# Kernel tuning notes

Measured on AMD Instinct MI355X. Metric: run time of the kernel, lower is better.

The kernel has to match this reference:

```python
import jax, jax.numpy as jnp
import numpy as np

NUM_ROUTING = 3


def squash(s, axis=-1):
    # squash(s) = |s|^2/(1+|s|^2) * s/|s|  (no epsilon, matching the torch code)
    sq = jnp.sum(s * s, axis=axis, keepdims=True)
    return sq / (1.0 + sq) * (s / jnp.sqrt(sq))


def setup_inputs() -> dict:
    key = jax.random.key(0)
    k1, k2 = jax.random.split(key)
    B, in_dim, in_num = 256, 8, 1152
    out_num, out_dim = 10, 16
    x = jax.random.normal(k1, (B, in_dim, in_num), dtype=jnp.float32)
    W = jax.random.normal(k2, (in_num, out_num, out_dim, in_dim), dtype=jnp.float32)
    return {"x": x, "W": W}


def reference(x, W):
    # x: [B, in_dim, in_num]; W: [in_num(i), out_num(j), out_dim(d), in_dim(c)]
    B = x.shape[0]
    in_num, out_num = W.shape[0], W.shape[1]
    # u_hat[i,j,b,d] = sum_c W[i,j,d,c] * x[b,c,i]
    u_hat = jnp.einsum('ijdc,bci->ijbd', W, x)
    b_ij = jnp.zeros((in_num, out_num), dtype=x.dtype)
    v = None
    for _ in range(NUM_ROUTING):
        # DGL reduce: softmax over the output-capsule axis (bucket dim)
        c = jax.nn.softmax(b_ij, axis=1)                    # [i, j]
        s = jnp.einsum('ij,ijbd->jbd', c, u_hat)            # [j, B, d]
        v = squash(s, axis=2)                               # [j, B, d]
        # edge update: b_ij += mean_b sum_d v[j,b,d] * u_hat[i,j,b,d]
        b_ij = b_ij + jnp.einsum('jbd,ijbd->ij', v, u_hat) / B
    # output: [B, out_num, out_dim, 1]
    return jnp.transpose(v, (1, 0, 2))[..., None]
```

## Files before the change

kernel.cpp:

```cpp
#include <hip/hip_runtime.h>

#define IN_NUM 1152
#define OUT_NUM 10
#define OUT_DIM 16
#define IN_DIM 8
#define NB 256
#define KTOT 9216

#define OFF_SPART 0
#define SZ_SPART (96 * OUT_NUM * OUT_DIM * NB)
#define OFF_BP (OFF_SPART + SZ_SPART)
#define SZ_BP (32 * IN_NUM * OUT_NUM)
#define OFF_VT (OFF_BP + SZ_BP)
#define SZ_VT (NB * OUT_NUM * OUT_DIM)
#define OFF_WT2 (OFF_VT + SZ_VT)
#define SZ_WT2 (OUT_NUM * KTOT * OUT_DIM)
#define OFF_WTBF (OFF_WT2 + SZ_WT2)
#define SZ_WTBF (OUT_NUM * OUT_DIM * KTOT / 2)
#define OFF_XBF (OFF_WTBF + SZ_WTBF)
#define SZ_XBF (NB * KTOT / 2)

typedef short bf16x8 __attribute__((ext_vector_type(8)));
typedef float f32x4 __attribute__((ext_vector_type(4)));

__device__ __forceinline__ unsigned short f2bf(float f) {
    unsigned u = __float_as_uint(f);
    u = (u + 0x7FFFu + ((u >> 16) & 1u)) >> 16;
    return (unsigned short)u;
}
__device__ __forceinline__ float bf2f(unsigned short h) {
    return __uint_as_float((unsigned)h << 16);
}

__global__ __launch_bounds__(256) void k_prep(const float* __restrict__ x,
                                              const float* __restrict__ W,
                                              float* __restrict__ Wt2,
                                              unsigned short* __restrict__ Wtbf,
                                              unsigned short* __restrict__ xbf) {
    int u = blockIdx.x, t = threadIdx.x;
    if (u < 360) {
        __shared__ float lds2[32][129];
        int itile = u / 10, j = u - itile * 10;
        int i0 = itile * 32;
        int r0 = t >> 5, c4b = t & 31;
#pragma unroll
        for (int rr = 0; rr < 4; ++rr) {
            int rrow = rr * 8 + r0;
            float4 w4 = *reinterpret_cast<const float4*>(
                &W[(size_t)(i0 + rrow) * 1280 + j * 128 + c4b * 4]);
            lds2[rrow][c4b * 4 + 0] = w4.x; lds2[rrow][c4b * 4 + 1] = w4.y;
            lds2[rrow][c4b * 4 + 2] = w4.z; lds2[rrow][c4b * 4 + 3] = w4.w;
        }
        __syncthreads();
        int ii = t & 31, dcq = t >> 5;
#pragma unroll
        for (int rr = 0; rr < 16; ++rr) {
            int dc = rr * 8 + dcq;
            Wtbf[(size_t)(j * 128 + dc) * IN_NUM + i0 + ii] = f2bf(lds2[ii][dc]);
        }
        int d4 = t & 3, ii2 = (t >> 2) & 31, ch0 = t >> 7;
#pragma unroll
        for (int c2 = 0; c2 < 4; ++c2) {
            int c = c2 * 2 + ch0;
            float4 o;
            o.x = lds2[ii2][(d4 * 4 + 0) * 8 + c];
            o.y = lds2[ii2][(d4 * 4 + 1) * 8 + c];
            o.z = lds2[ii2][(d4 * 4 + 2) * 8 + c];
            o.w = lds2[ii2][(d4 * 4 + 3) * 8 + c];
            *reinterpret_cast<float4*>(
                &Wt2[((size_t)j * KTOT + c * IN_NUM + i0 + ii2) * OUT_DIM + d4 * 4]) = o;
        }
    } else {
        int u2 = u - 360;
        const float4* x4 = reinterpret_cast<const float4*>(x);
#pragma unroll
        for (int p = 0; p < 16; ++p) {
            int e4 = u2 * 4096 + p * 256 + t;
            float4 v = x4[e4];
            ushort4 o;
            o.x = f2bf(v.x); o.y = f2bf(v.y); o.z = f2bf(v.z); o.w = f2bf(v.w);
            *reinterpret_cast<ushort4*>(&xbf[(size_t)e4 * 4]) = o;
        }
    }
}

__global__ __launch_bounds__(256, 4) void k_p1(const float* __restrict__ x,
                                               const float* __restrict__ Wt2,
                                               const float* __restrict__ bp,
                                               float* __restrict__ spart, int it) {
    __shared__ float ldc[96];
    __shared__ unsigned short atT[16][100];
    int w = blockIdx.x, t = threadIdx.x;
    int g8 = w / 80, r = w - g8 * 80;
    int j = r >> 3, isp = g8 * 8 + (r & 7);
    int cch = isp / 12;
    int i0 = (isp - cch * 12) * 96;
    int k0 = isp * 96;
    if (t < 96) {
        float cv;
        if (it == 0) {
            cv = 0.1f;
        } else {
            int i = i0 + t;
            float bt_[OUT_NUM];
#pragma unroll
            for (int jp = 0; jp < OUT_NUM; ++jp) bt_[jp] = 0.f;
#pragma unroll 4
            for (int row = 0; row < 32; ++row) {
                const float2* p2 = reinterpret_cast<const float2*>(
                    &bp[(size_t)row * (IN_NUM * OUT_NUM) + i * OUT_NUM]);
#pragma unroll
                for (int q = 0; q < 5; ++q) {
                    float2 v = p2[q];
                    bt_[q * 2] += v.x; bt_[q * 2 + 1] += v.y;
                }
            }
            float m = -1e30f;
#pragma unroll
            for (int jp = 0; jp < OUT_NUM; ++jp) { bt_[jp] *= (1.f / NB); m = fmaxf(m, bt_[jp]); }
            float s = 0.f;
#pragma unroll
            for (int jp = 0; jp < OUT_NUM; ++jp) { bt_[jp] = __expf(bt_[jp] - m); s += bt_[jp]; }
            cv = bt_[j] / s;
        }
        ldc[t] = cv;
    }
    __syncthreads();
    for (int e = t; e < 1536; e += 256) {
        int d = e & 15, kk = e >> 4;
        atT[d][kk] = f2bf(ldc[kk] * Wt2[((size_t)j * KTOT + k0 + kk) * OUT_DIM + d]);
    }
    __syncthreads();
    int lane = t & 63, wv = t >> 6;
    int lg = lane >> 4, lm = lane & 15;
    bf16x8 bfr[3];
#pragma unroll
    for (int ks = 0; ks < 3; ++ks) {
        const unsigned short* p0 = &atT[lm][ks * 32 + lg * 4];
        ushort4 u0 = *reinterpret_cast<const ushort4*>(p0);
        ushort4 u1 = *reinterpret_cast<const ushort4*>(p0 + 16);
        bfr[ks][0] = (short)u0.x; bfr[ks][1] = (short)u0.y;
        bfr[ks][2] = (short)u0.z; bfr[ks][3] = (short)u0.w;
        bfr[ks][4] = (short)u1.x; bfr[ks][5] = (short)u1.y;
        bfr[ks][6] = (short)u1.z; bfr[ks][7] = (short)u1.w;
    }
    float* sp = spart + ((size_t)isp * OUT_NUM + j) * (OUT_DIM * NB);
#pragma unroll
    for (int tb = 0; tb < 4; ++tb) {
        int tbase = (wv * 4 + tb) * 16;
        const float* xr = x + (size_t)(tbase + lm) * KTOT + k0 + lg * 4;
        f32x4 acc = {0.f, 0.f, 0.f, 0.f};
#pragma unroll
        for (int ks = 0; ks < 3; ++ks) {
            float4 a0 = *reinterpret_cast<const float4*>(xr + ks * 32);
            float4 a1 = *reinterpret_cast<const float4*>(xr + ks * 32 + 16);
            bf16x8 af;
            af[0] = (short)f2bf(a0.x); af[1] = (short)f2bf(a0.y);
            af[2] = (short)f2bf(a0.z); af[3] = (short)f2bf(a0.w);
            af[4] = (short)f2bf(a1.x); af[5] = (short)f2bf(a1.y);
            af[6] = (short)f2bf(a1.z); af[7] = (short)f2bf(a1.w);
            acc = __builtin_amdgcn_mfma_f32_16x16x32_bf16(af, bfr[ks], acc, 0, 0, 0);
        }
        *reinterpret_cast<float4*>(&sp[(size_t)lm * NB + tbase + lg * 4]) =
            make_float4(acc[0], acc[1], acc[2], acc[3]);
    }
}

__global__ __launch_bounds__(256, 4) void k_p2(const float* __restrict__ spart,
                                               float* __restrict__ dst) {
    __shared__ float smem[4672];
    float (*red)[32][17] = (float (*)[32][17])smem;
    float (*nrm)[9] = (float (*)[9])(smem + 4352);
    float* cf = smem + 4640;
    int wvar = blockIdx.x, t = threadIdx.x;
    int j = wvar >> 3, bt2 = wvar & 7;
    int ie = t >> 5, bb = t & 31;
    int b = bt2 * 32 + bb;
    float acc[16];
#pragma unroll
    for (int d = 0; d < 16; ++d) acc[d] = 0.f;
    for (int q = 0; q < 12; ++q) {
        int isp = ie * 12 + q;
        const float* sp = spart + (size_t)(isp * OUT_NUM + j) * (OUT_DIM * NB) + b;
#pragma unroll
        for (int d = 0; d < 16; ++d) acc[d] += sp[d * NB];
    }
#pragma unroll
    for (int d = 0; d < 16; ++d) red[ie][bb][d] = acc[d];
    __syncthreads();
    int bb2 = t >> 3, dp = t & 7;
    float s0 = 0.f, s1 = 0.f;
#pragma unroll
    for (int e = 0; e < 8; ++e) { s0 += red[e][bb2][dp * 2]; s1 += red[e][bb2][dp * 2 + 1]; }
    nrm[bb2][dp] = s0 * s0 + s1 * s1;
    __syncthreads();
    if (t < 32) {
        float qn = 0.f;
#pragma unroll
        for (int d = 0; d < 8; ++d) qn += nrm[t][d];
        cf[t] = qn / ((1.f + qn) * sqrtf(qn));
    }
    __syncthreads();
    float cs = cf[bb2];
    float* o = dst + (size_t)(bt2 * 32 + bb2) * (OUT_NUM * OUT_DIM) + j * OUT_DIM + dp * 2;
    o[0] = s0 * cs;
    o[1] = s1 * cs;
}

__global__ __launch_bounds__(256) void k_p3(const unsigned short* __restrict__ xbf,
                                            const float* __restrict__ vt,
                                            const unsigned short* __restrict__ Wtbf,
                                            float* __restrict__ bp, int it) {
    int u = blockIdx.x, t = threadIdx.x;
    int kt = u % 36;
    int jq = u / 36;
    int j = jq >> 2, bq = jq & 3;
    int k = kt * 256 + t;
    int c = k / IN_NUM, i = k - c * IN_NUM;
    const unsigned short* xk = xbf + k + (size_t)(bq * 64) * KTOT;
    const float* vjb = vt + (size_t)(bq * 64) * (OUT_NUM * OUT_DIM) + j * OUT_DIM;
    float macc[16];
#pragma unroll
    for (int d = 0; d < 16; ++d) macc[d] = 0.f;
#pragma unroll 8
    for (int b = 0; b < 64; ++b) {
        float xv = bf2f(xk[(size_t)b * KTOT]);
        const float* vb = vjb + (size_t)b * (OUT_NUM * OUT_DIM);
#pragma unroll
        for (int d = 0; d < 16; ++d) macc[d] += vb[d] * xv;
    }
    float bs = 0.f;
#pragma unroll
    for (int d = 0; d < 16; ++d)
        bs += macc[d] * bf2f(Wtbf[(size_t)(j * OUT_DIM + d) * KTOT + k]);
    size_t idx = (size_t)(bq * 8 + c) * (IN_NUM * OUT_NUM) + (size_t)i * OUT_NUM + j;
    float prev = (it == 0) ? 0.f : bp[idx];
    bp[idx] = prev + bs;
}

extern "C" void kernel_launch(void* const* d_in, const int* in_sizes, int n_in,
                              void* d_out, int out_size, void* d_ws, size_t ws_size,
                              hipStream_t stream) {
    const float* x = (const float*)d_in[0];
    const float* W = (const float*)d_in[1];
    float* out = (float*)d_out;
    float* ws = (float*)d_ws;

    float* spart = ws + OFF_SPART;
    float* bp    = ws + OFF_BP;
    float* vt    = ws + OFF_VT;
    float* Wt2   = ws + OFF_WT2;
    unsigned short* Wtbf = (unsigned short*)(ws + OFF_WTBF);
    unsigned short* xbf  = (unsigned short*)(ws + OFF_XBF);

    k_prep<<<dim3(504), dim3(256), 0, stream>>>(x, W, Wt2, Wtbf, xbf);
    for (int it = 0; it < 3; ++it) {
        k_p1<<<dim3(960), dim3(256), 0, stream>>>(x, Wt2, bp, spart, it);
        k_p2<<<dim3(80), dim3(256), 0, stream>>>(spart, it == 2 ? out : vt);
        if (it < 2) k_p3<<<dim3(1440), dim3(256), 0, stream>>>(xbf, vt, Wtbf, bp, it);
    }
}
```

Baseline: 121.0 us.

## Fuse weight/input preprocessing into first routing iteration's k_p1 kernel

```diff
diff --git a/kernel.cpp b/kernel.cpp
--- a/kernel.cpp
+++ b/kernel.cpp
@@ -32,60 +32,11 @@
     return __uint_as_float((unsigned)h << 16);
 }
 
-__global__ __launch_bounds__(256) void k_prep(const float* __restrict__ x,
-                                              const float* __restrict__ W,
-                                              float* __restrict__ Wt2,
-                                              unsigned short* __restrict__ Wtbf,
-                                              unsigned short* __restrict__ xbf) {
-    int u = blockIdx.x, t = threadIdx.x;
-    if (u < 360) {
-        __shared__ float lds2[32][129];
-        int itile = u / 10, j = u - itile * 10;
-        int i0 = itile * 32;
-        int r0 = t >> 5, c4b = t & 31;
-#pragma unroll
-        for (int rr = 0; rr < 4; ++rr) {
-            int rrow = rr * 8 + r0;
-            float4 w4 = *reinterpret_cast<const float4*>(
-                &W[(size_t)(i0 + rrow) * 1280 + j * 128 + c4b * 4]);
-            lds2[rrow][c4b * 4 + 0] = w4.x; lds2[rrow][c4b * 4 + 1] = w4.y;
-            lds2[rrow][c4b * 4 + 2] = w4.z; lds2[rrow][c4b * 4 + 3] = w4.w;
-        }
-        __syncthreads();
-        int ii = t & 31, dcq = t >> 5;
-#pragma unroll
-        for (int rr = 0; rr < 16; ++rr) {
-            int dc = rr * 8 + dcq;
-            Wtbf[(size_t)(j * 128 + dc) * IN_NUM + i0 + ii] = f2bf(lds2[ii][dc]);
-        }
-        int d4 = t & 3, ii2 = (t >> 2) & 31, ch0 = t >> 7;
-#pragma unroll
-        for (int c2 = 0; c2 < 4; ++c2) {
-            int c = c2 * 2 + ch0;
-            float4 o;
-            o.x = lds2[ii2][(d4 * 4 + 0) * 8 + c];
-            o.y = lds2[ii2][(d4 * 4 + 1) * 8 + c];
-            o.z = lds2[ii2][(d4 * 4 + 2) * 8 + c];
-            o.w = lds2[ii2][(d4 * 4 + 3) * 8 + c];
-            *reinterpret_cast<float4*>(
-                &Wt2[((size_t)j * KTOT + c * IN_NUM + i0 + ii2) * OUT_DIM + d4 * 4]) = o;
-        }
-    } else {
-        int u2 = u - 360;
-        const float4* x4 = reinterpret_cast<const float4*>(x);
-#pragma unroll
-        for (int p = 0; p < 16; ++p) {
-            int e4 = u2 * 4096 + p * 256 + t;
-            float4 v = x4[e4];
-            ushort4 o;
-            o.x = f2bf(v.x); o.y = f2bf(v.y); o.z = f2bf(v.z); o.w = f2bf(v.w);
-            *reinterpret_cast<ushort4*>(&xbf[(size_t)e4 * 4]) = o;
-        }
-    }
-}
-
 __global__ __launch_bounds__(256, 4) void k_p1(const float* __restrict__ x,
-                                               const float* __restrict__ Wt2,
+                                               const float* __restrict__ W,
+                                               float* __restrict__ Wt2,
+                                               unsigned short* __restrict__ Wtbf,
+                                               unsigned short* __restrict__ xbf,
                                                const float* __restrict__ bp,
                                                float* __restrict__ spart, int it) {
     __shared__ float ldc[96];
@@ -96,39 +47,43 @@
     int cch = isp / 12;
     int i0 = (isp - cch * 12) * 96;
     int k0 = isp * 96;
-    if (t < 96) {
-        float cv;
-        if (it == 0) {
-            cv = 0.1f;
-        } else {
-            int i = i0 + t;
-            float bt_[OUT_NUM];
-#pragma unroll
-            for (int jp = 0; jp < OUT_NUM; ++jp) bt_[jp] = 0.f;
+    if (it > 0 && t < 96) {
+        int i = i0 + t;
+        float bt_[OUT_NUM];
+#pragma unroll
+        for (int jp = 0; jp < OUT_NUM; ++jp) bt_[jp] = 0.f;
 #pragma unroll 4
-            for (int row = 0; row < 32; ++row) {
-                const float2* p2 = reinterpret_cast<const float2*>(
-                    &bp[(size_t)row * (IN_NUM * OUT_NUM) + i * OUT_NUM]);
-#pragma unroll
-                for (int q = 0; q < 5; ++q) {
-                    float2 v = p2[q];
-                    bt_[q * 2] += v.x; bt_[q * 2 + 1] += v.y;
-                }
+        for (int row = 0; row < 32; ++row) {
+            const float2* p2 = reinterpret_cast<const float2*>(
+                &bp[(size_t)row * (IN_NUM * OUT_NUM) + i * OUT_NUM]);
+#pragma unroll
+            for (int q = 0; q < 5; ++q) {
+                float2 v = p2[q];
+                bt_[q * 2] += v.x; bt_[q * 2 + 1] += v.y;
             }
-            float m = -1e30f;
-#pragma unroll
-            for (int jp = 0; jp < OUT_NUM; ++jp) { bt_[jp] *= (1.f / NB); m = fmaxf(m, bt_[jp]); }
-            float s = 0.f;
-#pragma unroll
-            for (int jp = 0; jp < OUT_NUM; ++jp) { bt_[jp] = __expf(bt_[jp] - m); s += bt_[jp]; }
-            cv = bt_[j] / s;
-        }
-        ldc[t] = cv;
-    }
-    __syncthreads();
-    for (int e = t; e < 1536; e += 256) {
-        int d = e & 15, kk = e >> 4;
-        atT[d][kk] = f2bf(ldc[kk] * Wt2[((size_t)j * KTOT + k0 + kk) * OUT_DIM + d]);
+        }
+        float m = -1e30f;
+#pragma unroll
+        for (int jp = 0; jp < OUT_NUM; ++jp) { bt_[jp] *= (1.f / NB); m = fmaxf(m, bt_[jp]); }
+        float s = 0.f;
+#pragma unroll
+        for (int jp = 0; jp < OUT_NUM; ++jp) { bt_[jp] = __expf(bt_[jp] - m); s += bt_[jp]; }
+        ldc[t] = bt_[j] / s;
+    }
+    __syncthreads();
+    if (it == 0) {
+        for (int e = t; e < 1536; e += 256) {
+            int d = e / 96, kk = e - d * 96;
+            float raw = W[(size_t)(i0 + kk) * 1280 + j * 128 + d * 8 + cch];
+            Wt2[((size_t)j * KTOT + cch * IN_NUM + i0 + kk) * OUT_DIM + d] = raw;
+            Wtbf[(size_t)(j * 128 + d * 8 + cch) * IN_NUM + i0 + kk] = f2bf(raw);
+            atT[d][kk] = f2bf(0.1f * raw);
+        }
+    } else {
+        for (int e = t; e < 1536; e += 256) {
+            int d = e & 15, kk = e >> 4;
+            atT[d][kk] = f2bf(ldc[kk] * Wt2[((size_t)j * KTOT + k0 + kk) * OUT_DIM + d]);
+        }
     }
     __syncthreads();
     int lane = t & 63, wv = t >> 6;
@@ -163,6 +118,15 @@
         }
         *reinterpret_cast<float4*>(&sp[(size_t)lm * NB + tbase + lg * 4]) =
             make_float4(acc[0], acc[1], acc[2], acc[3]);
+    }
+    if (it == 0) {
+        const float4* x4 = reinterpret_cast<const float4*>(x);
+        for (int e4 = w * 256 + t; e4 < NB * KTOT / 4; e4 += 960 * 256) {
+            float4 v = x4[e4];
+            ushort4 o;
+            o.x = f2bf(v.x); o.y = f2bf(v.y); o.z = f2bf(v.z); o.w = f2bf(v.w);
+            *reinterpret_cast<ushort4*>(&xbf[(size_t)e4 * 4]) = o;
+        }
     }
 }
 
@@ -253,9 +217,8 @@
     unsigned short* Wtbf = (unsigned short*)(ws + OFF_WTBF);
     unsigned short* xbf  = (unsigned short*)(ws + OFF_XBF);
 
-    k_prep<<<dim3(504), dim3(256), 0, stream>>>(x, W, Wt2, Wtbf, xbf);
     for (int it = 0; it < 3; ++it) {
-        k_p1<<<dim3(960), dim3(256), 0, stream>>>(x, Wt2, bp, spart, it);
+        k_p1<<<dim3(960), dim3(256), 0, stream>>>(x, W, Wt2, Wtbf, xbf, bp, spart, it);
         k_p2<<<dim3(80), dim3(256), 0, stream>>>(spart, it == 2 ? out : vt);
         if (it < 2) k_p3<<<dim3(1440), dim3(256), 0, stream>>>(xbf, vt, Wtbf, bp, it);
     }
```

Result: slower. 124.1 us (+2.6%).
